# Kernel tuning notes

Hardware: AMD Instinct MI355X
Metric: run time of the kernel (lower is better)

Reference implementation:

```python
import jax, jax.numpy as jnp
import numpy as np

B, S, DM = 2, 2048, 2048
H, DH = 16, 128
EPS = 1e-6


def rmsnorm(t, w):
    # normalize over last dim (head_dim), fp32 math
    var = jnp.mean(jnp.square(t), axis=-1, keepdims=True)
    return t * jax.lax.rsqrt(var + EPS) * w


def apply_rope(t, freqs):
    # t: (B,S,H,D); freqs: (S,1,D/2,2,2)
    b, s, h, d = t.shape
    t2 = t.reshape(b, s, h, 2, d // 2)
    t2 = jnp.moveaxis(t2, -2, -1)[..., None, :]  # (B,S,H,D/2,1,2)
    out = freqs[..., 0] * t2[..., 0] + freqs[..., 1] * t2[..., 1]  # (B,S,H,D/2,2)
    out = jnp.moveaxis(out, -1, -2).reshape(b, s, h, d)
    return out.astype(t.dtype)


def setup_inputs() -> dict:
    key = jax.random.key(0)
    ks = jax.random.split(key, 6)
    sc = 0.02
    return {
        "x": jax.random.normal(ks[0], (B, S, DM), jnp.float32),
        "rope_emb": jax.random.normal(ks[1], (S, 1, DH // 2, 2, 2), jnp.float32),
        "wq": jax.random.normal(ks[2], (DM, DM), jnp.float32) * sc,
        "wk": jax.random.normal(ks[3], (DM, DM), jnp.float32) * sc,
        "wv": jax.random.normal(ks[4], (DM, DM), jnp.float32) * sc,
        "wo": jax.random.normal(ks[5], (DM, DM), jnp.float32) * sc,
        "q_norm_w": jnp.ones((DH,), jnp.float32),
        "k_norm_w": jnp.ones((DH,), jnp.float32),
    }


def reference(x, rope_emb, wq, wk, wv, wo, q_norm_w, k_norm_w):
    b, s, _ = x.shape
    q = (x @ wq.T).reshape(b, s, H, DH)
    k = (x @ wk.T).reshape(b, s, H, DH)
    v = (x @ wv.T).reshape(b, s, H, DH)
    q = rmsnorm(q, q_norm_w)
    k = rmsnorm(k, k_norm_w)
    q = apply_rope(q, rope_emb)
    k = apply_rope(k, rope_emb)
    scale = 1.0 / np.sqrt(DH).astype(np.float32)
    scores = jnp.einsum('bqhd,bkhd->bhqk', q, k) * scale
    attn = jax.nn.softmax(scores, axis=-1)
    out = jnp.einsum('bhqk,bkhd->bqhd', attn, v).reshape(b, s, H * DH)
    return out @ wo.T
```

## Files before the change

kernel.cpp:

```cpp
#include <hip/hip_runtime.h>

typedef __bf16 bf16x8 __attribute__((ext_vector_type(8)));
typedef __bf16 bf16x4 __attribute__((ext_vector_type(4)));
typedef float floatx4 __attribute__((ext_vector_type(4)));

#define GK 2048
#define S_LEN 2048
#define NH 16
#define DH 128
#define NKT (GK / 64)

__device__ __forceinline__ void gl2lds16c(const __bf16* g, char* l) {
    __builtin_amdgcn_global_load_lds(
        (const __attribute__((address_space(1))) void*)g,
        (__attribute__((address_space(3))) void*)l, 16, 0, 0);
}

__global__ __launch_bounds__(256) void cvt_bf16(const float* __restrict__ in,
                                                __bf16* __restrict__ out, int n4) {
    int i = blockIdx.x * 256 + threadIdx.x;
    if (i < n4) {
        const float4 v = ((const float4*)in)[i];
        bf16x4 h;
        h[0] = (__bf16)v.x; h[1] = (__bf16)v.y; h[2] = (__bf16)v.z; h[3] = (__bf16)v.w;
        ((bf16x4*)out)[i] = h;
    }
}

__global__ __launch_bounds__(256) void cvt3_bf16(const float* __restrict__ a,
                                                 const float* __restrict__ b,
                                                 const float* __restrict__ c,
                                                 __bf16* __restrict__ out) {
    const int per = 2048 * 2048 / 4;
    int i = blockIdx.x * 256 + threadIdx.x;
    const float* src = a; int j = i;
    if (i >= 2 * per)      { src = c; j = i - 2 * per; }
    else if (i >= per)     { src = b; j = i - per; }
    const float4 v = ((const float4*)src)[j];
    bf16x4 h;
    h[0] = (__bf16)v.x; h[1] = (__bf16)v.y; h[2] = (__bf16)v.z; h[3] = (__bf16)v.w;
    ((bf16x4*)out)[i] = h;
}

__device__ __forceinline__ int xcd_remap(int L, int nwg) {
    return (L & 7) * (nwg >> 3) + (L >> 3);
}

__device__ __forceinline__ void gemm_body5(const __bf16* __restrict__ A,
                                           const __bf16* __restrict__ W,
                                           int m0, int n0, char* lds,
                                           floatx4 (*acc)[3]) {
    const int t = threadIdx.x, l = t & 63, wave = t >> 6;
    const int fr = l & 15, fq = l >> 4;
    const int wm = wave >> 2, wn = wave & 3;

    const int swcol = ((l & 7) * 8) ^ (((l >> 3) & 7) * 8);
    const __bf16* gA = A + (size_t)(m0 + wave * 8 + (l >> 3)) * GK + swcol;
    const __bf16* gW = W + (size_t)(n0 + wave * 8 + (l >> 3)) * GK + swcol;
    char* const ldsW = lds + wave * 1024;

    auto stageA = [&](int p, int kt, int q) {
        gl2lds16c(gA + (size_t)q * 64 * GK + kt * 64,
                  ldsW + p * 57344 + q * 8192);
    };
    auto stageBh = [&](int p, int kt, int h) {
        gl2lds16c(gW + (size_t)h * 64 * GK + kt * 64,
                  ldsW + p * 57344 + 32768 + h * 8192);
    };

#pragma unroll
    for (int q = 0; q < 4; q++) stageA(0, 0, q);
#pragma unroll
    for (int h = 0; h < 3; h++) stageBh(0, 0, h);
#pragma unroll
    for (int q = 0; q < 4; q++) stageA(1, 1, q);
#pragma unroll
    for (int h = 0; h < 3; h++) stageBh(1, 1, h);

    const int sw = (fr & 7) << 4;
    const int cb0 = (fq * 16) ^ sw;
    const int cb1 = (64 + fq * 16) ^ sw;

    for (int t0 = 0; t0 < NKT; t0++) {
        const int p = t0 & 1;
        if (t0 == NKT - 1) { asm volatile("s_waitcnt vmcnt(0)" ::: "memory"); }
        else               { asm volatile("s_waitcnt vmcnt(7)" ::: "memory"); }
        __builtin_amdgcn_s_barrier();
        asm volatile("" ::: "memory");

        const char* bufA = lds + p * 57344;
        const char* bufB = bufA + 32768;

        bf16x8 bB[3][2];
#pragma unroll
        for (int j = 0; j < 3; j++) {
            const char* rb = bufB + (wn * 48 + j * 16 + fr) * 128;
            bB[j][0] = *(const bf16x8*)(rb + cb0);
            bB[j][1] = *(const bf16x8*)(rb + cb1);
        }
        bf16x8 af[2][2][2];
        {
            const char* ra = bufA + (wm * 32 + fr) * 128;
#pragma unroll
            for (int i = 0; i < 2; i++) {
                af[0][i][0] = *(const bf16x8*)(ra + i * 2048 + cb0);
                af[0][i][1] = *(const bf16x8*)(ra + i * 2048 + cb1);
            }
        }

#pragma unroll
        for (int q = 0; q < 4; q++) {
            if (t0 + 2 < NKT) {
                if (q == 1) { stageA(p, t0 + 2, 0); stageBh(p, t0 + 2, 0); stageBh(p, t0 + 2, 1); }
                if (q == 2) { stageA(p, t0 + 2, 1); stageBh(p, t0 + 2, 2); }
                if (q == 3) { stageA(p, t0 + 2, 2); }
            }
            if (q < 3) {
                const char* ra = bufA + ((q + 1) * 64 + wm * 32 + fr) * 128;
#pragma unroll
                for (int i = 0; i < 2; i++) {
                    af[(q + 1) & 1][i][0] = *(const bf16x8*)(ra + i * 2048 + cb0);
                    af[(q + 1) & 1][i][1] = *(const bf16x8*)(ra + i * 2048 + cb1);
                }
            }
            __builtin_amdgcn_s_setprio(1);
#pragma unroll
            for (int i = 0; i < 2; i++)
#pragma unroll
                for (int j = 0; j < 3; j++) {
                    acc[2 * q + i][j] = __builtin_amdgcn_mfma_f32_16x16x32_bf16(af[q & 1][i][0], bB[j][0], acc[2 * q + i][j], 0, 0, 0);
                    acc[2 * q + i][j] = __builtin_amdgcn_mfma_f32_16x16x32_bf16(af[q & 1][i][1], bB[j][1], acc[2 * q + i][j], 0, 0, 0);
                }
            __builtin_amdgcn_s_setprio(0);
            __builtin_amdgcn_s_barrier();
            asm volatile("" ::: "memory");
        }
        if (t0 + 2 < NKT) stageA(p, t0 + 2, 3);
    }
}

__device__ __forceinline__ void gemm_body4(const __bf16* __restrict__ A,
                                           const __bf16* __restrict__ W,
                                           int m0, int n0, char* lds,
                                           floatx4 (*acc)[4]) {
    const int t = threadIdx.x, l = t & 63, wave = t >> 6;
    const int fr = l & 15, fq = l >> 4;
    const int wm = wave >> 2, wn = wave & 3;

    const int swcol = ((l & 7) * 8) ^ (((l >> 3) & 7) * 8);
    const __bf16* gA = A + (size_t)(m0 + wave * 8 + (l >> 3)) * GK + swcol;
    const __bf16* gW = W + (size_t)(n0 + wave * 8 + (l >> 3)) * GK + swcol;
    char* const ldsW = lds + wave * 1024;

    auto stageA = [&](int p, int kt, int c) {
        gl2lds16c(gA + (size_t)c * 64 * GK + kt * 64,
                  ldsW + p * 49152 + c * 8192);
    };
    auto stageBh = [&](int p, int kt, int h) {
        gl2lds16c(gW + (size_t)h * 64 * GK + kt * 64,
                  ldsW + p * 49152 + 16384 + h * 8192);
    };

    stageA(0, 0, 0); stageA(0, 0, 1);
#pragma unroll
    for (int h = 0; h < 4; h++) stageBh(0, 0, h);
    stageA(1, 1, 0); stageA(1, 1, 1);
#pragma unroll
    for (int h = 0; h < 4; h++) stageBh(1, 1, h);

    const int sw = (fr & 7) << 4;
    const int cb0 = (fq * 16) ^ sw;
    const int cb1 = (64 + fq * 16) ^ sw;

    for (int t0 = 0; t0 < NKT; t0++) {
        const int p = t0 & 1;
        if (t0 == NKT - 1) { asm volatile("s_waitcnt vmcnt(0)" ::: "memory"); }
        else               { asm volatile("s_waitcnt vmcnt(6)" ::: "memory"); }
        __builtin_amdgcn_s_barrier();
        asm volatile("" ::: "memory");

        const char* bufA = lds + p * 49152;
        const char* bufB = bufA + 16384;

        bf16x8 bB[4][2];
#pragma unroll
        for (int j = 0; j < 4; j++) {
            const char* rb = bufB + (wn * 64 + j * 16 + fr) * 128;
            bB[j][0] = *(const bf16x8*)(rb + cb0);
            bB[j][1] = *(const bf16x8*)(rb + cb1);
        }
        bf16x8 af[2][2];
        {
            const char* ra = bufA + (wm * 16 + fr) * 128;
            af[0][0] = *(const bf16x8*)(ra + cb0);
            af[0][1] = *(const bf16x8*)(ra + cb1);
        }

#pragma unroll
        for (int q = 0; q < 4; q++) {
            if (t0 + 2 < NKT) {
                if (q == 1) { stageBh(p, t0 + 2, 0); stageBh(p, t0 + 2, 1); }
                if (q == 2) { stageBh(p, t0 + 2, 2); stageBh(p, t0 + 2, 3); stageA(p, t0 + 2, 0); }
            }
            if (q < 3) {
                const char* ra = bufA + ((q + 1) * 32 + wm * 16 + fr) * 128;
                af[(q + 1) & 1][0] = *(const bf16x8*)(ra + cb0);
                af[(q + 1) & 1][1] = *(const bf16x8*)(ra + cb1);
            }
            __builtin_amdgcn_s_setprio(1);
#pragma unroll
            for (int j = 0; j < 4; j++) {
                acc[q][j] = __builtin_amdgcn_mfma_f32_16x16x32_bf16(af[q & 1][0], bB[j][0], acc[q][j], 0, 0, 0);
                acc[q][j] = __builtin_amdgcn_mfma_f32_16x16x32_bf16(af[q & 1][1], bB[j][1], acc[q][j], 0, 0, 0);
            }
            __builtin_amdgcn_s_setprio(0);
            __builtin_amdgcn_s_barrier();
            asm volatile("" ::: "memory");
        }
        if (t0 + 2 < NKT) stageA(p, t0 + 2, 1);
    }
}

__global__ __launch_bounds__(512, 2) void gemm_qkv(const __bf16* __restrict__ A,
                                                   const __bf16* __restrict__ W,
                                                   __bf16* __restrict__ qb,
                                                   __bf16* __restrict__ kb,
                                                   __bf16* __restrict__ vbT) {
    extern __shared__ __align__(16) char lds[];
    const int gx = gridDim.x;
    const int L = blockIdx.x + gx * blockIdx.y;
    const int tid2 = xcd_remap(L, gx * (int)gridDim.y);
    const int m0 = (tid2 / gx) * 256, n0 = (tid2 % gx) * 192;
    floatx4 acc[8][3] = {};
    gemm_body5(A, W, m0, n0, lds, acc);

    const int lane = threadIdx.x & 63, wave = threadIdx.x >> 6;
    const int fr = lane & 15, fq = lane >> 4;
    const int wm = wave >> 2, wn = wave & 3;

    for (int mi = 0; mi < 8; mi++)
        for (int j = 0; j < 3; j++) {
            const int row = m0 + (mi >> 1) * 64 + wm * 32 + (mi & 1) * 16 + fq * 4;
            const int c0 = n0 + wn * 48 + j * 16;
            const int which = c0 >> 11;
            const int col = (c0 & 2047) + fr;
            if (which == 2) {
                __bf16* Cp = vbT + (((size_t)(row & ~2047)) << 11) +
                             (size_t)col * 2048 + (row & 2047);
                bf16x4 hv;
                for (int r = 0; r < 4; r++) hv[r] = (__bf16)acc[mi][j][r];
                *(bf16x4*)Cp = hv;
            } else {
                __bf16* dst = which ? kb : qb;
                for (int r = 0; r < 4; r++)
                    dst[(size_t)(row + r) * 2048 + col] = (__bf16)acc[mi][j][r];
            }
        }
}

__global__ __launch_bounds__(512, 2) void gemm_out(const __bf16* __restrict__ A,
                                                   const __bf16* __restrict__ W,
                                                   float* __restrict__ C) {
    extern __shared__ __align__(16) char lds[];
    const int gx = gridDim.x;
    const int L = blockIdx.x + gx * blockIdx.y;
    const int tid2 = xcd_remap(L, gx * (int)gridDim.y);
    const int m0 = (tid2 / gx) * 128, n0 = (tid2 % gx) * 256;
    floatx4 acc[4][4] = {};
    gemm_body4(A, W, m0, n0, lds, acc);

    const int lane = threadIdx.x & 63, wave = threadIdx.x >> 6;
    const int fr = lane & 15, fq = lane >> 4;
    const int wm = wave >> 2, wn = wave & 3;
    for (int mi = 0; mi < 4; mi++)
        for (int j = 0; j < 4; j++) {
            const int row = m0 + mi * 32 + wm * 16 + fq * 4;
            const int col = n0 + wn * 64 + j * 16 + fr;
            for (int r = 0; r < 4; r++)
                C[(size_t)(row + r) * 2048 + col] = acc[mi][j][r];
        }
}

__global__ __launch_bounds__(256) void rmsrope(__bf16* __restrict__ qb,
                                               __bf16* __restrict__ kb,
                                               const float* __restrict__ rope,
                                               const float* __restrict__ qw,
                                               const float* __restrict__ kw) {
    const int lane = threadIdx.x & 63;
    const int row = blockIdx.x * 4 + (threadIdx.x >> 6);
    __bf16* p = (blockIdx.y ? kb : qb) + (size_t)row * DH;
    const float* w = blockIdx.y ? kw : qw;
    const int s = (row >> 4) & (S_LEN - 1);

    float t0 = (float)p[lane];
    float t1 = (float)p[lane + 64];
    float ss = t0 * t0 + t1 * t1;
    for (int o = 32; o; o >>= 1) ss += __shfl_xor(ss, o, 64);
    const float inv = rsqrtf(ss * (1.0f / 128.0f) + 1e-6f);
    t0 *= inv * w[lane];
    t1 *= inv * w[lane + 64];

    const float4 f = *(const float4*)(rope + (size_t)s * 256 + lane * 4);
    p[lane]      = (__bf16)(f.x * t0 + f.y * t1);
    p[lane + 64] = (__bf16)(f.z * t0 + f.w * t1);
}

__global__ __launch_bounds__(256, 2) void flash(const __bf16* __restrict__ Q,
                                                const __bf16* __restrict__ K,
                                                const __bf16* __restrict__ Vt_g,
                                                __bf16* __restrict__ O) {
    extern __shared__ __align__(16) char lds[];

    const int t = threadIdx.x, lane = t & 63, wave = t >> 6;
    const int fr = lane & 15, fq = lane >> 4;

    const int n = blockIdx.x + (int)gridDim.x * blockIdx.y;
    const int by = (n & 7) * 4 + (n >> 7);
    const int bx = (n >> 3) & 15;
    const int b = by >> 4, h = by & 15;

    const size_t baseQ = (size_t)b * S_LEN * 2048 + h * 128;
    const size_t baseV = (size_t)b * 2048 * 2048 + (size_t)h * 128 * 2048;
    const int q0 = bx * 128 + wave * 32;
    const float sc2 = 0.08838834764831845f * 1.4426950408889634f;
    const float M2 = 12.0f * 1.4426950408889634f;

    bf16x8 qf[2][4];
#pragma unroll
    for (int i2 = 0; i2 < 2; i2++) {
        const __bf16* qp = Q + baseQ + (size_t)(q0 + i2 * 16 + fr) * 2048 + fq * 8;
#pragma unroll
        for (int c = 0; c < 4; c++) qf[i2][c] = *(const bf16x8*)(qp + c * 32);
    }
    asm volatile("s_waitcnt vmcnt(0)" ::: "memory");

    bf16x8 onesb;
#pragma unroll
    for (int e = 0; e < 8; e++) onesb[e] = (__bf16)1.0f;

    const int l4 = lane >> 4;
    const int c16 = lane & 15;
    const int l3 = lane >> 3;
    const int c8 = lane & 7;
    const __bf16* gK0 = K + baseQ + (size_t)(wave * 16 + l4) * 2048 + (c16 ^ l4) * 8;
    const __bf16* gK1 = K + baseQ + (size_t)(wave * 16 + l4) * 2048 + (c16 ^ (4 + l4)) * 8;
    const __bf16* gV  = Vt_g + baseV + (size_t)(wave * 8 + l3) * 2048 + (c8 ^ l3) * 8;

    char* const kdw = lds + wave * 4096;
    char* const vdw = lds + 32768 + wave * 1024;

    auto stage = [&](int p, int it2) {
        const size_t ko = (size_t)it2 * 64 * 2048;
        char* kd = kdw + p * 16384;
        gl2lds16c(gK0 + ko,                      kd);
        gl2lds16c(gK1 + ko + (size_t)4 * 2048,   kd + 1024);
        gl2lds16c(gK0 + ko + (size_t)8 * 2048,   kd + 2048);
        gl2lds16c(gK1 + ko + (size_t)12 * 2048,  kd + 3072);
        const __bf16* v = gV + it2 * 64;
        char* vd = vdw + p * 16384;
        gl2lds16c(v,                        vd);
        gl2lds16c(v + (size_t)32 * 2048,    vd + 4096);
        gl2lds16c(v + (size_t)64 * 2048,    vd + 8192);
        gl2lds16c(v + (size_t)96 * 2048,    vd + 12288);
    };

    stage(0, 0);
    stage(1, 1);

    floatx4 oa[2][9] = {};
    char* const Pw = lds + 65536 + wave * 4096;
    const int sw = (fr & 7) << 4;

    for (int it = 0; it < 32; ++it) {
        const int p = it & 1;
        if (it == 31) { asm volatile("s_waitcnt vmcnt(0)" ::: "memory"); }
        else          { asm volatile("s_waitcnt vmcnt(8)" ::: "memory"); }
        __builtin_amdgcn_s_barrier();
        asm volatile("" ::: "memory");

        const char* Kb = lds + p * 16384;
        const char* Vb = lds + 32768 + p * 16384;

        floatx4 sacc[2][4] = {};
#pragma unroll
        for (int j = 0; j < 4; j++) {
            const char* kr = Kb + (j * 16 + fr) * 256;
            const bf16x8 kf0 = *(const bf16x8*)(kr + ((0 + fq * 16) ^ sw));
            const bf16x8 kf1 = *(const bf16x8*)(kr + ((64 + fq * 16) ^ sw));
            const bf16x8 kf2 = *(const bf16x8*)(kr + ((128 + fq * 16) ^ sw));
            const bf16x8 kf3 = *(const bf16x8*)(kr + ((192 + fq * 16) ^ sw));
            __builtin_amdgcn_s_setprio(1);
            sacc[0][j] = __builtin_amdgcn_mfma_f32_16x16x32_bf16(qf[0][0], kf0, sacc[0][j], 0, 0, 0);
            sacc[1][j] = __builtin_amdgcn_mfma_f32_16x16x32_bf16(qf[1][0], kf0, sacc[1][j], 0, 0, 0);
            sacc[0][j] = __builtin_amdgcn_mfma_f32_16x16x32_bf16(qf[0][1], kf1, sacc[0][j], 0, 0, 0);
            sacc[1][j] = __builtin_amdgcn_mfma_f32_16x16x32_bf16(qf[1][1], kf1, sacc[1][j], 0, 0, 0);
            sacc[0][j] = __builtin_amdgcn_mfma_f32_16x16x32_bf16(qf[0][2], kf2, sacc[0][j], 0, 0, 0);
            sacc[1][j] = __builtin_amdgcn_mfma_f32_16x16x32_bf16(qf[1][2], kf2, sacc[1][j], 0, 0, 0);
            sacc[0][j] = __builtin_amdgcn_mfma_f32_16x16x32_bf16(qf[0][3], kf3, sacc[0][j], 0, 0, 0);
            sacc[1][j] = __builtin_amdgcn_mfma_f32_16x16x32_bf16(qf[1][3], kf3, sacc[1][j], 0, 0, 0);
            __builtin_amdgcn_s_setprio(0);
        }

#pragma unroll
        for (int i2 = 0; i2 < 2; i2++)
#pragma unroll
            for (int r = 0; r < 4; r++) {
                const int row = i2 * 16 + fq * 4 + r;
                char* pr = Pw + row * 128;
                const int rsw = ((fq * 4 + r) & 7) << 4;
#pragma unroll
                for (int j = 0; j < 4; j++)
                    *(__bf16*)(pr + ((j * 32 + fr * 2) ^ rsw)) =
                        (__bf16)exp2f(fmaf(sc2, sacc[i2][j][r], -M2));
            }

        bf16x8 pf[2][2];
#pragma unroll
        for (int i2 = 0; i2 < 2; i2++) {
            const char* pr = Pw + (i2 * 16 + fr) * 128;
            pf[i2][0] = *(const bf16x8*)(pr + ((fq * 16) ^ sw));
            pf[i2][1] = *(const bf16x8*)(pr + ((64 + fq * 16) ^ sw));
        }
#pragma unroll
        for (int nb = 0; nb < 8; nb++) {
            const char* vr = Vb + (nb * 16 + fr) * 128;
            const bf16x8 vf0 = *(const bf16x8*)(vr + ((fq * 16) ^ sw));
            const bf16x8 vf1 = *(const bf16x8*)(vr + ((64 + fq * 16) ^ sw));
            __builtin_amdgcn_s_setprio(1);
            oa[0][nb] = __builtin_amdgcn_mfma_f32_16x16x32_bf16(pf[0][0], vf0, oa[0][nb], 0, 0, 0);
            oa[1][nb] = __builtin_amdgcn_mfma_f32_16x16x32_bf16(pf[1][0], vf0, oa[1][nb], 0, 0, 0);
            oa[0][nb] = __builtin_amdgcn_mfma_f32_16x16x32_bf16(pf[0][1], vf1, oa[0][nb], 0, 0, 0);
            oa[1][nb] = __builtin_amdgcn_mfma_f32_16x16x32_bf16(pf[1][1], vf1, oa[1][nb], 0, 0, 0);
            __builtin_amdgcn_s_setprio(0);
        }
        oa[0][8] = __builtin_amdgcn_mfma_f32_16x16x32_bf16(pf[0][0], onesb, oa[0][8], 0, 0, 0);
        oa[1][8] = __builtin_amdgcn_mfma_f32_16x16x32_bf16(pf[1][0], onesb, oa[1][8], 0, 0, 0);
        oa[0][8] = __builtin_amdgcn_mfma_f32_16x16x32_bf16(pf[0][1], onesb, oa[0][8], 0, 0, 0);
        oa[1][8] = __builtin_amdgcn_mfma_f32_16x16x32_bf16(pf[1][1], onesb, oa[1][8], 0, 0, 0);

        __builtin_amdgcn_s_barrier();
        asm volatile("" ::: "memory");
        if (it < 30) stage(p, it + 2);
    }

    for (int i2 = 0; i2 < 2; i2++)
        for (int r = 0; r < 4; r++) {
            const float inv = 1.0f / oa[i2][8][r];
            __bf16* op = O + baseQ + (size_t)(q0 + i2 * 16 + fq * 4 + r) * 2048;
            for (int nb = 0; nb < 8; nb++)
                op[nb * 16 + fr] = (__bf16)(oa[i2][nb][r] * inv);
        }
}

extern "C" void kernel_launch(void* const* d_in, const int* in_sizes, int n_in,
                              void* d_out, int out_size, void* d_ws, size_t ws_size,
                              hipStream_t stream) {
    const float* x    = (const float*)d_in[0];
    const float* rope = (const float*)d_in[1];
    const float* wq   = (const float*)d_in[2];
    const float* wk   = (const float*)d_in[3];
    const float* wv   = (const float*)d_in[4];
    const float* wo   = (const float*)d_in[5];
    const float* qnw  = (const float*)d_in[6];
    const float* knw  = (const float*)d_in[7];
    float* out = (float*)d_out;

    static bool attr_set = false;
    if (!attr_set) {
        hipFuncSetAttribute((const void*)gemm_qkv,
                            hipFuncAttributeMaxDynamicSharedMemorySize, 114688);
        hipFuncSetAttribute((const void*)gemm_out,
                            hipFuncAttributeMaxDynamicSharedMemorySize, 98304);
        hipFuncSetAttribute((const void*)flash,
                            hipFuncAttributeMaxDynamicSharedMemorySize, 81920);
        attr_set = true;
    }

    const size_t NTOK = 2 * 2048;
    const size_t ELEMS = NTOK * 2048;
    __bf16* xb  = (__bf16*)d_ws;
    __bf16* qb  = xb + ELEMS;
    __bf16* kb  = qb + ELEMS;
    __bf16* vbT = kb + ELEMS;
    __bf16* ob  = xb;
    __bf16* wqkv = (__bf16*)d_out;
    __bf16* wob  = qb;

    cvt_bf16<<<(int)(ELEMS / 4) / 256, 256, 0, stream>>>(x, xb, (int)(ELEMS / 4));
    cvt3_bf16<<<3 * (2048 * 2048 / 4) / 256, 256, 0, stream>>>(wq, wk, wv, wqkv);
    gemm_qkv<<<dim3(6144 / 192, (unsigned)(NTOK / 256)), 512, 114688, stream>>>(xb, wqkv, qb, kb, vbT);
    rmsrope<<<dim3((unsigned)(NTOK * 16 / 4), 2), 256, 0, stream>>>(qb, kb, rope, qnw, knw);
    flash<<<dim3(S_LEN / 128, 2 * 16), 256, 81920, stream>>>(qb, kb, vbT, ob);
    cvt_bf16<<<(int)(2048 * 2048 / 4) / 256, 256, 0, stream>>>(wo, wob, 2048 * 2048 / 4);
    gemm_out<<<dim3(2048 / 256, (unsigned)(NTOK / 128)), 512, 98304, stream>>>(ob, wob, out);
}
```

Measured before the change: 420.5 us.

## Keep softmax P tile in registers via transposed MFMA and ds_bpermute

Result: faster. 382.3 us (-9.1%).

```diff
diff --git a/kernel.cpp b/kernel.cpp
--- a/kernel.cpp
+++ b/kernel.cpp
@@ -3,6 +3,7 @@
 typedef __bf16 bf16x8 __attribute__((ext_vector_type(8)));
 typedef __bf16 bf16x4 __attribute__((ext_vector_type(4)));
 typedef float floatx4 __attribute__((ext_vector_type(4)));
+typedef unsigned int uintx4 __attribute__((ext_vector_type(4)));
 
 #define GK 2048
 #define S_LEN 2048
@@ -368,8 +369,10 @@
     stage(1, 1);
 
     floatx4 oa[2][9] = {};
-    char* const Pw = lds + 65536 + wave * 4096;
     const int sw = (fr & 7) << 4;
+    const int il0 = (fr + 16 * (2 * (fq & 1))) * 4;
+    const int il1 = il0 + 64;
+    const bool jhi = (fq >> 1) != 0;
 
     for (int it = 0; it < 32; ++it) {
         const int p = it & 1;
@@ -390,37 +393,53 @@
             const bf16x8 kf2 = *(const bf16x8*)(kr + ((128 + fq * 16) ^ sw));
             const bf16x8 kf3 = *(const bf16x8*)(kr + ((192 + fq * 16) ^ sw));
             __builtin_amdgcn_s_setprio(1);
-            sacc[0][j] = __builtin_amdgcn_mfma_f32_16x16x32_bf16(qf[0][0], kf0, sacc[0][j], 0, 0, 0);
-            sacc[1][j] = __builtin_amdgcn_mfma_f32_16x16x32_bf16(qf[1][0], kf0, sacc[1][j], 0, 0, 0);
-            sacc[0][j] = __builtin_amdgcn_mfma_f32_16x16x32_bf16(qf[0][1], kf1, sacc[0][j], 0, 0, 0);
-            sacc[1][j] = __builtin_amdgcn_mfma_f32_16x16x32_bf16(qf[1][1], kf1, sacc[1][j], 0, 0, 0);
-            sacc[0][j] = __builtin_amdgcn_mfma_f32_16x16x32_bf16(qf[0][2], kf2, sacc[0][j], 0, 0, 0);
-            sacc[1][j] = __builtin_amdgcn_mfma_f32_16x16x32_bf16(qf[1][2], kf2, sacc[1][j], 0, 0, 0);
-            sacc[0][j] = __builtin_amdgcn_mfma_f32_16x16x32_bf16(qf[0][3], kf3, sacc[0][j], 0, 0, 0);
-            sacc[1][j] = __builtin_amdgcn_mfma_f32_16x16x32_bf16(qf[1][3], kf3, sacc[1][j], 0, 0, 0);
+            sacc[0][j] = __builtin_amdgcn_mfma_f32_16x16x32_bf16(kf0, qf[0][0], sacc[0][j], 0, 0, 0);
+            sacc[1][j] = __builtin_amdgcn_mfma_f32_16x16x32_bf16(kf0, qf[1][0], sacc[1][j], 0, 0, 0);
+            sacc[0][j] = __builtin_amdgcn_mfma_f32_16x16x32_bf16(kf1, qf[0][1], sacc[0][j], 0, 0, 0);
+            sacc[1][j] = __builtin_amdgcn_mfma_f32_16x16x32_bf16(kf1, qf[1][1], sacc[1][j], 0, 0, 0);
+            sacc[0][j] = __builtin_amdgcn_mfma_f32_16x16x32_bf16(kf2, qf[0][2], sacc[0][j], 0, 0, 0);
+            sacc[1][j] = __builtin_amdgcn_mfma_f32_16x16x32_bf16(kf2, qf[1][2], sacc[1][j], 0, 0, 0);
+            sacc[0][j] = __builtin_amdgcn_mfma_f32_16x16x32_bf16(kf3, qf[0][3], sacc[0][j], 0, 0, 0);
+            sacc[1][j] = __builtin_amdgcn_mfma_f32_16x16x32_bf16(kf3, qf[1][3], sacc[1][j], 0, 0, 0);
             __builtin_amdgcn_s_setprio(0);
         }
 
+        unsigned int pk2[2][4][2];
 #pragma unroll
         for (int i2 = 0; i2 < 2; i2++)
 #pragma unroll
-            for (int r = 0; r < 4; r++) {
-                const int row = i2 * 16 + fq * 4 + r;
-                char* pr = Pw + row * 128;
-                const int rsw = ((fq * 4 + r) & 7) << 4;
-#pragma unroll
-                for (int j = 0; j < 4; j++)
-                    *(__bf16*)(pr + ((j * 32 + fr * 2) ^ rsw)) =
-                        (__bf16)exp2f(fmaf(sc2, sacc[i2][j][r], -M2));
+            for (int j = 0; j < 4; j++) {
+                float pv[4];
+#pragma unroll
+                for (int r = 0; r < 4; r++)
+                    pv[r] = exp2f(fmaf(sc2, sacc[i2][j][r], -M2));
+                asm("v_cvt_pk_bf16_f32 %0, %1, %2"
+                    : "=v"(pk2[i2][j][0]) : "v"(pv[0]), "v"(pv[1]));
+                asm("v_cvt_pk_bf16_f32 %0, %1, %2"
+                    : "=v"(pk2[i2][j][1]) : "v"(pv[2]), "v"(pv[3]));
             }
 
         bf16x8 pf[2][2];
 #pragma unroll
-        for (int i2 = 0; i2 < 2; i2++) {
-            const char* pr = Pw + (i2 * 16 + fr) * 128;
-            pf[i2][0] = *(const bf16x8*)(pr + ((fq * 16) ^ sw));
-            pf[i2][1] = *(const bf16x8*)(pr + ((64 + fq * 16) ^ sw));
-        }
+        for (int i2 = 0; i2 < 2; i2++)
+#pragma unroll
+            for (int kc = 0; kc < 2; kc++) {
+                uintx4 w;
+                const unsigned int a0 = __builtin_amdgcn_ds_bpermute(il0, pk2[i2][2 * kc][0]);
+                const unsigned int b0 = __builtin_amdgcn_ds_bpermute(il0, pk2[i2][2 * kc + 1][0]);
+                const unsigned int a1 = __builtin_amdgcn_ds_bpermute(il0, pk2[i2][2 * kc][1]);
+                const unsigned int b1 = __builtin_amdgcn_ds_bpermute(il0, pk2[i2][2 * kc + 1][1]);
+                const unsigned int a2 = __builtin_amdgcn_ds_bpermute(il1, pk2[i2][2 * kc][0]);
+                const unsigned int b2 = __builtin_amdgcn_ds_bpermute(il1, pk2[i2][2 * kc + 1][0]);
+                const unsigned int a3 = __builtin_amdgcn_ds_bpermute(il1, pk2[i2][2 * kc][1]);
+                const unsigned int b3 = __builtin_amdgcn_ds_bpermute(il1, pk2[i2][2 * kc + 1][1]);
+                w[0] = jhi ? b0 : a0;
+                w[1] = jhi ? b1 : a1;
+                w[2] = jhi ? b2 : a2;
+                w[3] = jhi ? b3 : a3;
+                pf[i2][kc] = *(const bf16x8*)&w;
+            }
+
 #pragma unroll
         for (int nb = 0; nb < 8; nb++) {
             const char* vr = Vb + (nb * 16 + fr) * 128;
@@ -472,7 +491,7 @@
         hipFuncSetAttribute((const void*)gemm_out,
                             hipFuncAttributeMaxDynamicSharedMemorySize, 98304);
         hipFuncSetAttribute((const void*)flash,
-                            hipFuncAttributeMaxDynamicSharedMemorySize, 81920);
+                            hipFuncAttributeMaxDynamicSharedMemorySize, 65536);
         attr_set = true;
     }
 
@@ -490,7 +509,7 @@
     cvt3_bf16<<<3 * (2048 * 2048 / 4) / 256, 256, 0, stream>>>(wq, wk, wv, wqkv);
     gemm_qkv<<<dim3(6144 / 192, (unsigned)(NTOK / 256)), 512, 114688, stream>>>(xb, wqkv, qb, kb, vbT);
     rmsrope<<<dim3((unsigned)(NTOK * 16 / 4), 2), 256, 0, stream>>>(qb, kb, rope, qnw, knw);
-    flash<<<dim3(S_LEN / 128, 2 * 16), 256, 81920, stream>>>(qb, kb, vbT, ob);
+    flash<<<dim3(S_LEN / 128, 2 * 16), 256, 65536, stream>>>(qb, kb, vbT, ob);
     cvt_bf16<<<(int)(2048 * 2048 / 4) / 256, 256, 0, stream>>>(wo, wob, 2048 * 2048 / 4);
     gemm_out<<<dim3(2048 / 256, (unsigned)(NTOK / 128)), 512, 98304, stream>>>(ob, wob, out);
 }
```
